# Performance work log

Measured on AMD Instinct MI355X. Metric: run time of the kernel, lower is better.

## Reference

```python
import jax, jax.numpy as jnp
import numpy as np

H = 1024
V = 32000
L = 15
B = 512


def setup_inputs() -> dict:
    key = jax.random.key(0)
    ks = jax.random.split(key, 16)
    s = 0.02
    return {
        "input_ids": jax.random.randint(ks[0], (B,), 0, V),
        "hidden": jax.random.normal(ks[1], (1, B, H), jnp.float32),
        "encoder_outputs": jax.random.normal(ks[2], (L, B, H), jnp.float32),
        "max_length": L,
        "embedding": jax.random.normal(ks[3], (V, H), jnp.float32) * s,
        "attn1_w": jax.random.normal(ks[4], (1, 2 * H), jnp.float32) * s,
        "attn1_b": jnp.zeros((1,), jnp.float32),
        "combine_w": jax.random.normal(ks[5], (H, 2 * H), jnp.float32) * s,
        "combine_b": jnp.zeros((H,), jnp.float32),
        "w_ih": jax.random.normal(ks[6], (3 * H, H), jnp.float32) * s,
        "w_hh": jax.random.normal(ks[7], (3 * H, H), jnp.float32) * s,
        "b_ih": jnp.zeros((3 * H,), jnp.float32),
        "b_hh": jnp.zeros((3 * H,), jnp.float32),
        "out_w": jax.random.normal(ks[8], (V, H), jnp.float32) * s,
        "out_b": jnp.zeros((V,), jnp.float32),
    }


def reference(input_ids, hidden, encoder_outputs, max_length, embedding,
              attn1_w, attn1_b, combine_w, combine_b,
              w_ih, w_hh, b_ih, b_hh, out_w, out_b):
    # embedding lookup (dropout is identity in eval mode)
    emb = embedding[input_ids]                       # [B, H]
    # Bahdanau-style additive scores: vectorize the per-step python loop
    emb_l = jnp.broadcast_to(emb[None], (max_length, B, H))   # [L, B, H]
    cat = jnp.concatenate([emb_l, encoder_outputs], axis=-1)  # [L, B, 2H]
    scores = cat @ attn1_w.T + attn1_b               # [L, B, 1]
    attn_weights = jax.nn.softmax(scores, axis=0)    # softmax over L
    ctx = jnp.sum(attn_weights * encoder_outputs, axis=0)     # [B, H]
    x = jnp.concatenate([emb, ctx], axis=-1) @ combine_w.T + combine_b  # [B, H]
    # n_layers = 1: relu then one GRU step (seq len 1)
    x = jax.nn.relu(x)
    h = hidden[0]                                    # [B, H]
    gi = x @ w_ih.T + b_ih                           # [B, 3H]
    gh = h @ w_hh.T + b_hh                           # [B, 3H]
    i_r, i_z, i_n = jnp.split(gi, 3, axis=1)
    h_r, h_z, h_n = jnp.split(gh, 3, axis=1)
    r = jax.nn.sigmoid(i_r + h_r)
    z = jax.nn.sigmoid(i_z + h_z)
    n = jnp.tanh(i_n + r * h_n)
    h_new = (1.0 - z) * n + z * h                    # [B, H]
    logits = h_new @ out_w.T + out_b                 # [B, V]
    output = jax.nn.log_softmax(logits, axis=1)
    return output, h_new[None], attn_weights
```

## Files before the change

### kernel.cpp

```cpp
#include <hip/hip_runtime.h>

#define HH 1024
#define VV 32000
#define LL 15
#define BB 512

typedef __bf16 bf16;
typedef __bf16 bf16x4 __attribute__((ext_vector_type(4)));
typedef __bf16 bf16x8 __attribute__((ext_vector_type(8)));
typedef float f32x4 __attribute__((ext_vector_type(4)));

__device__ __forceinline__ unsigned short f2bf(float f) {
    unsigned int u = __float_as_uint(f);
    unsigned int r = (u + 0x7fffu + ((u >> 16) & 1u)) >> 16;
    return (unsigned short)r;
}

__device__ __forceinline__ void gld_lds16(const void* g, void* l) {
    __builtin_amdgcn_global_load_lds(
        (const __attribute__((address_space(1))) unsigned int*)g,
        (__attribute__((address_space(3))) unsigned int*)l, 16, 0, 0);
}

__global__ __launch_bounds__(256)
void cvt4_kernel(const float* __restrict__ a0, unsigned short* __restrict__ o0, int n0_,
                 const float* __restrict__ a1, unsigned short* __restrict__ o1, int n1_,
                 const float* __restrict__ a2, unsigned short* __restrict__ o2, int n2_,
                 const float* __restrict__ a3, unsigned short* __restrict__ o3, int n3_) {
    int i = blockIdx.x * 256 + threadIdx.x;
    const float* src; unsigned short* dst;
    if (i < n0_) { src = a0; dst = o0; }
    else if ((i -= n0_) < n1_) { src = a1; dst = o1; }
    else if ((i -= n1_) < n2_) { src = a2; dst = o2; }
    else if ((i -= n2_) < n3_) { src = a3; dst = o3; }
    else return;
    const f32x4 a = ((const f32x4*)src)[2 * i], b = ((const f32x4*)src)[2 * i + 1];
    ((bf16x4*)dst)[2 * i]     = __builtin_convertvector(a, bf16x4);
    ((bf16x4*)dst)[2 * i + 1] = __builtin_convertvector(b, bf16x4);
}

__global__ __launch_bounds__(256)
void attn_kernel(const int* __restrict__ ids, const float* __restrict__ enc,
                 const float* __restrict__ embedding,
                 const float* __restrict__ attn1_w, const float* __restrict__ attn1_b,
                 float* __restrict__ attn_out, unsigned short* __restrict__ cat_out) {
    const int b = blockIdx.x, tid = threadIdx.x;
    const int lane = tid & 63, wv = tid >> 6;

    __shared__ float s_enc[LL * HH];
    __shared__ float s_scores[LL];
    __shared__ float s_red[4];

    for (int idx = tid; idx < LL * HH / 4; idx += 256) {
        const int l = (idx * 4) >> 10, h = (idx * 4) & (HH - 1);
        *(f32x4*)&s_enc[idx * 4] = *(const f32x4*)&enc[((size_t)l * BB + b) * HH + h];
    }

    const float* embr = embedding + (size_t)ids[b] * HH;
    float p = 0.f;
    for (int j = tid; j < HH; j += 256) p += embr[j] * attn1_w[j];
    #pragma unroll
    for (int o = 32; o; o >>= 1) p += __shfl_xor(p, o);
    if (lane == 0) s_red[wv] = p;
    __syncthreads();
    const float semb = s_red[0] + s_red[1] + s_red[2] + s_red[3] + attn1_b[0];

    for (int l = wv; l < LL; l += 4) {
        float q = 0.f;
        for (int j = lane; j < HH; j += 64) q += s_enc[l * HH + j] * attn1_w[HH + j];
        #pragma unroll
        for (int o = 32; o; o >>= 1) q += __shfl_xor(q, o);
        if (lane == 0) s_scores[l] = q + semb;
    }
    __syncthreads();

    float mx = -3.4e38f;
    #pragma unroll
    for (int l = 0; l < LL; l++) mx = fmaxf(mx, s_scores[l]);
    float aw[LL], sum = 0.f;
    #pragma unroll
    for (int l = 0; l < LL; l++) { aw[l] = __expf(s_scores[l] - mx); sum += aw[l]; }
    const float inv = 1.f / sum;
    #pragma unroll
    for (int l = 0; l < LL; l++) aw[l] *= inv;

    if (tid < LL) attn_out[tid * BB + b] = aw[tid];

    for (int j = tid; j < HH; j += 256) {
        float c = 0.f;
        #pragma unroll
        for (int l = 0; l < LL; l++) c += aw[l] * s_enc[l * HH + j];
        cat_out[(size_t)b * (2 * HH) + j] = f2bf(embr[j]);
        cat_out[(size_t)b * (2 * HH) + HH + j] = f2bf(c);
    }
}

template<int TM, int TN, int OUT, int GATES>
__global__ __launch_bounds__(256)
void gemm_nt(const bf16* __restrict__ A, const bf16* __restrict__ B,
             const float* __restrict__ bias, void* __restrict__ Cout,
             const bf16* __restrict__ A2, const bf16* __restrict__ B2,
             const float* __restrict__ bias2, void* __restrict__ C2,
             const int K, const int N) {
    constexpr int FM = TM / 32, FN = TN / 32;
    __shared__ bf16 As[TM * 64];
    __shared__ bf16 Bs[TN * 64];

    if (GATES && blockIdx.z == 1) { A = A2; B = B2; bias = bias2; Cout = C2; }

    const int tid = threadIdx.x;
    const int lane = tid & 63, wave = tid >> 6;
    const int wm = wave >> 1, wn = wave & 1;
    const int rlo = lane & 15, khi = lane >> 4;
    const int m0 = blockIdx.y * TM, n0 = blockIdx.x * TN;

    f32x4 acc[FM][FN] = {};
    constexpr int IA = TM / 32, IB = TN / 32;

    for (int k0 = 0; k0 < K; k0 += 64) {
        #pragma unroll
        for (int i = 0; i < IA; i++) {
            const int t = (i * 256 + tid) * 8;
            gld_lds16(A + (size_t)(m0 + (t >> 6)) * K + (k0 + (t & 63)), As + i * 2048 + wave * 512);
        }
        #pragma unroll
        for (int i = 0; i < IB; i++) {
            const int t = (i * 256 + tid) * 8;
            gld_lds16(B + (size_t)(n0 + (t >> 6)) * K + (k0 + (t & 63)), Bs + i * 2048 + wave * 512);
        }
        __syncthreads();

        bf16x8 af[FM][2], bfr[FN][2];
        #pragma unroll
        for (int m = 0; m < FM; m++)
            #pragma unroll
            for (int ks = 0; ks < 2; ks++)
                af[m][ks] = *(const bf16x8*)(As + (wm * (TM / 2) + m * 16 + rlo) * 64 + ks * 32 + khi * 8);
        #pragma unroll
        for (int n = 0; n < FN; n++)
            #pragma unroll
            for (int ks = 0; ks < 2; ks++)
                bfr[n][ks] = *(const bf16x8*)(Bs + (wn * (TN / 2) + n * 16 + rlo) * 64 + ks * 32 + khi * 8);
        #pragma unroll
        for (int ks = 0; ks < 2; ks++)
            #pragma unroll
            for (int m = 0; m < FM; m++)
                #pragma unroll
                for (int n = 0; n < FN; n++)
                    acc[m][n] = __builtin_amdgcn_mfma_f32_16x16x32_bf16(af[m][ks], bfr[n][ks], acc[m][n], 0, 0, 0);
        __syncthreads();
    }

    #pragma unroll
    for (int m = 0; m < FM; m++) {
        const int gr = m0 + wm * (TM / 2) + m * 16 + khi * 4;
        #pragma unroll
        for (int n = 0; n < FN; n++) {
            const int gc = n0 + wn * (TN / 2) + n * 16 + rlo;
            const float bv = bias[gc];
            #pragma unroll
            for (int j = 0; j < 4; j++) {
                float v = acc[m][n][j] + bv;
                if (OUT == 1) {
                    v = fmaxf(v, 0.f);
                    ((unsigned short*)Cout)[(size_t)(gr + j) * N + gc] = f2bf(v);
                } else {
                    ((float*)Cout)[(size_t)(gr + j) * N + gc] = v;
                }
            }
        }
    }
}

__global__ __launch_bounds__(256)
void gemm_out(const bf16* __restrict__ A, const float* __restrict__ B,
              const float* __restrict__ bias, float* __restrict__ C,
              float* __restrict__ pmax, float* __restrict__ psum) {
    constexpr int K = HH, N = VV;
    __shared__ bf16 As[128 * 64];
    __shared__ char BsB[128 * 128] __attribute__((aligned(128)));
    __shared__ float sPm[2][128], sPs[2][128];

    const int tid = threadIdx.x;
    const int lane = tid & 63, wave = tid >> 6;
    const int wm = wave >> 1, wn = wave & 1;
    const int rlo = lane & 15, khi = lane >> 4;

    constexpr int gridN = VV / 128;
    constexpr int nFull = (gridN >> 3) << 5;
    const int bidx = blockIdx.x;
    int g, jm;
    if (bidx < nFull) { const int s = bidx >> 5, rem = bidx & 31; jm = rem >> 3; g = s * 8 + (rem & 7); }
    else { const int rem = bidx - nFull; constexpr int gleft = gridN & 7; g = (gridN & ~7) + rem % gleft; jm = rem / gleft; }
    const int n0 = g * 128, m0 = jm * 128;

    f32x4 acc[4][4] = {};

    for (int k0 = 0; k0 < K; k0 += 64) {
        #pragma unroll
        for (int i = 0; i < 4; i++) {
            const int t = (i * 256 + tid) * 8;
            gld_lds16(A + (size_t)(m0 + (t >> 6)) * K + (k0 + (t & 63)), As + i * 2048 + wave * 512);
        }
        f32x4 bv[8];
        #pragma unroll
        for (int i = 0; i < 8; i++) {
            const int idx = i * 256 + tid;
            const int row = idx >> 4, c4 = idx & 15;
            bv[i] = *(const f32x4*)(B + (size_t)(n0 + row) * K + k0 + c4 * 4);
        }
        #pragma unroll
        for (int i = 0; i < 8; i++) {
            const int idx = i * 256 + tid;
            const int row = idx >> 4;
            bf16x4 w = __builtin_convertvector(bv[i], bf16x4);
            *(bf16x4*)(BsB + ((idx * 8) ^ ((row & 7) << 4))) = w;
        }
        __syncthreads();

        bf16x8 af[4][2], bfr[4][2];
        #pragma unroll
        for (int m = 0; m < 4; m++)
            #pragma unroll
            for (int ks = 0; ks < 2; ks++)
                af[m][ks] = *(const bf16x8*)(As + (wm * 64 + m * 16 + rlo) * 64 + ks * 32 + khi * 8);
        #pragma unroll
        for (int n = 0; n < 4; n++) {
            const int row = wn * 64 + n * 16 + rlo;
            #pragma unroll
            for (int ks = 0; ks < 2; ks++)
                bfr[n][ks] = *(const bf16x8*)(BsB + ((row * 128 + ks * 64 + khi * 16) ^ ((row & 7) << 4)));
        }
        #pragma unroll
        for (int ks = 0; ks < 2; ks++)
            #pragma unroll
            for (int m = 0; m < 4; m++)
                #pragma unroll
                for (int n = 0; n < 4; n++)
                    acc[m][n] = __builtin_amdgcn_mfma_f32_16x16x32_bf16(af[m][ks], bfr[n][ks], acc[m][n], 0, 0, 0);
        __syncthreads();
    }

    float bvn[4];
    #pragma unroll
    for (int n = 0; n < 4; n++) bvn[n] = bias[n0 + wn * 64 + n * 16 + rlo];

    #pragma unroll
    for (int m = 0; m < 4; m++) {
        const int rbase = wm * 64 + m * 16 + khi * 4;
        #pragma unroll
        for (int j = 0; j < 4; j++) {
            const int gr = m0 + rbase + j;
            float v[4];
            float lm = -3.4e38f;
            #pragma unroll
            for (int n = 0; n < 4; n++) {
                v[n] = acc[m][n][j] + bvn[n];
                C[(size_t)gr * N + n0 + wn * 64 + n * 16 + rlo] = v[n];
                lm = fmaxf(lm, v[n]);
            }
            #pragma unroll
            for (int o = 8; o; o >>= 1) lm = fmaxf(lm, __shfl_xor(lm, o));
            float ls = 0.f;
            #pragma unroll
            for (int n = 0; n < 4; n++) ls += __expf(v[n] - lm);
            #pragma unroll
            for (int o = 8; o; o >>= 1) ls += __shfl_xor(ls, o);
            if (rlo == 0) { sPm[wn][rbase + j] = lm; sPs[wn][rbase + j] = ls; }
        }
    }
    __syncthreads();
    if (tid < 128) {
        const float ma = sPm[0][tid], mb = sPm[1][tid];
        const float M = fmaxf(ma, mb);
        const float S = sPs[0][tid] * __expf(ma - M) + sPs[1][tid] * __expf(mb - M);
        pmax[(size_t)(m0 + tid) * 256 + g] = M;
        psum[(size_t)(m0 + tid) * 256 + g] = S;
    }
}

__global__ __launch_bounds__(256)
void gru_kernel(const float* __restrict__ gi, const float* __restrict__ gh,
                const float* __restrict__ h, float* __restrict__ hnew,
                unsigned short* __restrict__ hnew_bf) {
    const int i = blockIdx.x * 256 + threadIdx.x;
    const int e = i * 4;
    const int b = e >> 10, j = e & (HH - 1);
    const size_t o = ((size_t)b * 3 * HH + j) / 4;
    const f32x4 ir = ((const f32x4*)gi)[o],          iz = ((const f32x4*)gi)[o + HH / 4],
                in_ = ((const f32x4*)gi)[o + 2 * HH / 4];
    const f32x4 hr = ((const f32x4*)gh)[o],          hz = ((const f32x4*)gh)[o + HH / 4],
                hn = ((const f32x4*)gh)[o + 2 * HH / 4];
    const f32x4 hv = ((const f32x4*)h)[i];
    f32x4 out;
    ushort4 ob;
    #pragma unroll
    for (int c = 0; c < 4; c++) {
        const float r = 1.f / (1.f + __expf(-(ir[c] + hr[c])));
        const float z = 1.f / (1.f + __expf(-(iz[c] + hz[c])));
        const float n = tanhf(in_[c] + r * hn[c]);
        const float v = (1.f - z) * n + z * hv[c];
        out[c] = v;
        ((unsigned short*)&ob)[c] = f2bf(v);
    }
    ((f32x4*)hnew)[i] = out;
    ((ushort4*)hnew_bf)[i] = ob;
}

__global__ __launch_bounds__(256)
void lsm_final(const float* __restrict__ pmax, const float* __restrict__ psum,
               float* __restrict__ logits) {
    const int b = blockIdx.x, tid = threadIdx.x;
    const int lane = tid & 63, wv = tid >> 6;
    __shared__ float sm[4], ss[4];

    float m = -3.4e38f, s = 0.f;
    if (tid < VV / 128) { m = pmax[(size_t)b * 256 + tid]; s = psum[(size_t)b * 256 + tid]; }
    #pragma unroll
    for (int o = 32; o; o >>= 1) {
        const float mo = __shfl_xor(m, o), so = __shfl_xor(s, o);
        const float nm = fmaxf(m, mo);
        s = s * __expf(m - nm) + so * __expf(mo - nm);
        m = nm;
    }
    if (lane == 0) { sm[wv] = m; ss[wv] = s; }
    __syncthreads();
    const float M = fmaxf(fmaxf(sm[0], sm[1]), fmaxf(sm[2], sm[3]));
    const float S = ss[0] * __expf(sm[0] - M) + ss[1] * __expf(sm[1] - M)
                  + ss[2] * __expf(sm[2] - M) + ss[3] * __expf(sm[3] - M);
    const float lse = M + __logf(S);

    float* row = logits + (size_t)b * VV;
    for (int j = tid; j < VV / 4; j += 256) {
        f32x4 v = ((const f32x4*)row)[j];
        v[0] -= lse; v[1] -= lse; v[2] -= lse; v[3] -= lse;
        ((f32x4*)row)[j] = v;
    }
}

extern "C" void kernel_launch(void* const* d_in, const int* in_sizes, int n_in,
                              void* d_out, int out_size, void* d_ws, size_t ws_size,
                              hipStream_t stream) {
    const int*   ids       = (const int*)d_in[0];
    const float* hidden    = (const float*)d_in[1];
    const float* enc       = (const float*)d_in[2];
    const float* embedding = (const float*)d_in[4];
    const float* attn1_w   = (const float*)d_in[5];
    const float* attn1_b   = (const float*)d_in[6];
    const float* combine_w = (const float*)d_in[7];
    const float* combine_b = (const float*)d_in[8];
    const float* w_ih      = (const float*)d_in[9];
    const float* w_hh      = (const float*)d_in[10];
    const float* b_ih      = (const float*)d_in[11];
    const float* b_hh      = (const float*)d_in[12];
    const float* out_w     = (const float*)d_in[13];
    const float* out_b     = (const float*)d_in[14];

    float* out_lsm = (float*)d_out;
    float* out_h   = out_lsm + (size_t)BB * VV;
    float* out_aw  = out_h + (size_t)BB * HH;

    char* w = (char*)d_ws;
    unsigned short* w_ih_bf  = (unsigned short*)w;   w += (size_t)3 * HH * HH * 2;
    unsigned short* w_hh_bf  = (unsigned short*)w;   w += (size_t)3 * HH * HH * 2;
    unsigned short* w_cb_bf  = (unsigned short*)w;   w += (size_t)2 * HH * HH * 2;
    unsigned short* cat_bf   = (unsigned short*)w;   w += (size_t)BB * 2 * HH * 2;
    unsigned short* x_bf     = (unsigned short*)w;   w += (size_t)BB * HH * 2;
    unsigned short* hid_bf   = (unsigned short*)w;   w += (size_t)BB * HH * 2;
    unsigned short* hnew_bf  = (unsigned short*)w;   w += (size_t)BB * HH * 2;
    float* gi   = (float*)w;                         w += (size_t)BB * 3 * HH * 4;
    float* gh   = (float*)w;                         w += (size_t)BB * 3 * HH * 4;
    float* pmax = (float*)w;                         w += (size_t)BB * 256 * 4;
    float* psum = (float*)w;                         w += (size_t)BB * 256 * 4;

    cvt4_kernel<<<(3 * HH * HH / 8 * 2 + 2 * HH * HH / 8 + BB * HH / 8) / 256, 256, 0, stream>>>(
        w_ih, w_ih_bf, 3 * HH * HH / 8,
        w_hh, w_hh_bf, 3 * HH * HH / 8,
        combine_w, w_cb_bf, 2 * HH * HH / 8,
        hidden, hid_bf, BB * HH / 8);

    attn_kernel<<<BB, 256, 0, stream>>>(ids, enc, embedding, attn1_w, attn1_b, out_aw, cat_bf);

    gemm_nt<64, 64, 1, 0><<<dim3(HH / 64, BB / 64), 256, 0, stream>>>(
        (const bf16*)cat_bf, (const bf16*)w_cb_bf, combine_b, x_bf,
        nullptr, nullptr, nullptr, nullptr, 2 * HH, HH);

    gemm_nt<64, 64, 0, 1><<<dim3(3 * HH / 64, BB / 64, 2), 256, 0, stream>>>(
        (const bf16*)hid_bf, (const bf16*)w_hh_bf, b_hh, gh,
        (const bf16*)x_bf, (const bf16*)w_ih_bf, b_ih, gi, HH, 3 * HH);

    gru_kernel<<<(BB * HH / 4) / 256, 256, 0, stream>>>(gi, gh, hidden, out_h, hnew_bf);

    gemm_out<<<(VV / 128) * 4, 256, 0, stream>>>(
        (const bf16*)hnew_bf, out_w, out_b, out_lsm, pmax, psum);

    lsm_final<<<BB, 256, 0, stream>>>(pmax, psum, out_lsm);
}
```

Baseline: 186.0 us.

## Halve output GEMM N-tile to 64, swizzle A in LDS, widen softmax reduction

The vocabulary projection GEMM now uses 128x64 tiles instead of 128x128, which doubles the block count to 2000 and cuts per-thread accumulators, and it sets launch bounds to allow 3 blocks per CU. The A tile is now loaded into LDS with an XOR swizzle so fragment reads avoid bank conflicts. The partial max/sum buffers and the final log-softmax kernel are widened to 500 partials per row, using 512 threads. The aim is better occupancy and load balance on the largest GEMM, at the cost of re-reading the A tile twice as often and converting each fp32 weight tile from global memory with less reuse.

```diff
diff --git a/kernel.cpp b/kernel.cpp
--- a/kernel.cpp
+++ b/kernel.cpp
@@ -172,13 +172,13 @@
     }
 }
 
-__global__ __launch_bounds__(256)
+__global__ __launch_bounds__(256, 3)
 void gemm_out(const bf16* __restrict__ A, const float* __restrict__ B,
               const float* __restrict__ bias, float* __restrict__ C,
               float* __restrict__ pmax, float* __restrict__ psum) {
     constexpr int K = HH, N = VV;
     __shared__ bf16 As[128 * 64];
-    __shared__ char BsB[128 * 128] __attribute__((aligned(128)));
+    __shared__ bf16 Bs[64 * 64];
     __shared__ float sPm[2][128], sPs[2][128];
 
     const int tid = threadIdx.x;
@@ -186,64 +186,68 @@
     const int wm = wave >> 1, wn = wave & 1;
     const int rlo = lane & 15, khi = lane >> 4;
 
-    constexpr int gridN = VV / 128;
+    constexpr int gridN = VV / 64;
     constexpr int nFull = (gridN >> 3) << 5;
     const int bidx = blockIdx.x;
     int g, jm;
     if (bidx < nFull) { const int s = bidx >> 5, rem = bidx & 31; jm = rem >> 3; g = s * 8 + (rem & 7); }
     else { const int rem = bidx - nFull; constexpr int gleft = gridN & 7; g = (gridN & ~7) + rem % gleft; jm = rem / gleft; }
-    const int n0 = g * 128, m0 = jm * 128;
-
-    f32x4 acc[4][4] = {};
+    const int n0 = g * 64, m0 = jm * 128;
+
+    f32x4 acc[4][2] = {};
 
     for (int k0 = 0; k0 < K; k0 += 64) {
+        f32x4 bv[4];
         #pragma unroll
         for (int i = 0; i < 4; i++) {
-            const int t = (i * 256 + tid) * 8;
-            gld_lds16(A + (size_t)(m0 + (t >> 6)) * K + (k0 + (t & 63)), As + i * 2048 + wave * 512);
-        }
-        f32x4 bv[8];
-        #pragma unroll
-        for (int i = 0; i < 8; i++) {
             const int idx = i * 256 + tid;
             const int row = idx >> 4, c4 = idx & 15;
             bv[i] = *(const f32x4*)(B + (size_t)(n0 + row) * K + k0 + c4 * 4);
         }
         #pragma unroll
-        for (int i = 0; i < 8; i++) {
+        for (int i = 0; i < 4; i++) {
+            const int p = (i * 256 + tid) * 16;
+            const int row = p >> 7;
+            const int qs = (p & 127) ^ ((row & 7) << 4);
+            gld_lds16(A + (size_t)(m0 + row) * K + k0 + (qs >> 1),
+                      As + i * 2048 + wave * 512);
+        }
+        #pragma unroll
+        for (int i = 0; i < 4; i++) {
             const int idx = i * 256 + tid;
-            const int row = idx >> 4;
+            const int row = idx >> 4, c4 = idx & 15;
             bf16x4 w = __builtin_convertvector(bv[i], bf16x4);
-            *(bf16x4*)(BsB + ((idx * 8) ^ ((row & 7) << 4))) = w;
+            *(bf16x4*)((char*)Bs + row * 128 + ((c4 * 8) ^ ((row & 7) << 4))) = w;
         }
         __syncthreads();
 
-        bf16x8 af[4][2], bfr[4][2];
-        #pragma unroll
-        for (int m = 0; m < 4; m++)
-            #pragma unroll
-            for (int ks = 0; ks < 2; ks++)
-                af[m][ks] = *(const bf16x8*)(As + (wm * 64 + m * 16 + rlo) * 64 + ks * 32 + khi * 8);
-        #pragma unroll
-        for (int n = 0; n < 4; n++) {
-            const int row = wn * 64 + n * 16 + rlo;
-            #pragma unroll
-            for (int ks = 0; ks < 2; ks++)
-                bfr[n][ks] = *(const bf16x8*)(BsB + ((row * 128 + ks * 64 + khi * 16) ^ ((row & 7) << 4)));
-        }
-        #pragma unroll
-        for (int ks = 0; ks < 2; ks++)
+        #pragma unroll
+        for (int ks = 0; ks < 2; ks++) {
+            bf16x8 af[4], bfr[2];
+            #pragma unroll
+            for (int m = 0; m < 4; m++) {
+                const int r = wm * 64 + m * 16 + rlo;
+                const int sw = (ks * 64 + khi * 16) ^ ((r & 7) << 4);
+                af[m] = *(const bf16x8*)((const char*)As + r * 128 + sw);
+            }
+            #pragma unroll
+            for (int n = 0; n < 2; n++) {
+                const int r = wn * 32 + n * 16 + rlo;
+                const int sw = (ks * 64 + khi * 16) ^ ((r & 7) << 4);
+                bfr[n] = *(const bf16x8*)((const char*)Bs + r * 128 + sw);
+            }
             #pragma unroll
             for (int m = 0; m < 4; m++)
                 #pragma unroll
-                for (int n = 0; n < 4; n++)
-                    acc[m][n] = __builtin_amdgcn_mfma_f32_16x16x32_bf16(af[m][ks], bfr[n][ks], acc[m][n], 0, 0, 0);
+                for (int n = 0; n < 2; n++)
+                    acc[m][n] = __builtin_amdgcn_mfma_f32_16x16x32_bf16(af[m], bfr[n], acc[m][n], 0, 0, 0);
+        }
         __syncthreads();
     }
 
-    float bvn[4];
-    #pragma unroll
-    for (int n = 0; n < 4; n++) bvn[n] = bias[n0 + wn * 64 + n * 16 + rlo];
+    float bvn[2];
+    #pragma unroll
+    for (int n = 0; n < 2; n++) bvn[n] = bias[n0 + wn * 32 + n * 16 + rlo];
 
     #pragma unroll
     for (int m = 0; m < 4; m++) {
@@ -251,19 +255,16 @@
         #pragma unroll
         for (int j = 0; j < 4; j++) {
             const int gr = m0 + rbase + j;
-            float v[4];
-            float lm = -3.4e38f;
-            #pragma unroll
-            for (int n = 0; n < 4; n++) {
+            float v[2];
+            #pragma unroll
+            for (int n = 0; n < 2; n++) {
                 v[n] = acc[m][n][j] + bvn[n];
-                C[(size_t)gr * N + n0 + wn * 64 + n * 16 + rlo] = v[n];
-                lm = fmaxf(lm, v[n]);
+                C[(size_t)gr * N + n0 + wn * 32 + n * 16 + rlo] = v[n];
             }
+            float lm = fmaxf(v[0], v[1]);
             #pragma unroll
             for (int o = 8; o; o >>= 1) lm = fmaxf(lm, __shfl_xor(lm, o));
-            float ls = 0.f;
-            #pragma unroll
-            for (int n = 0; n < 4; n++) ls += __expf(v[n] - lm);
+            float ls = __expf(v[0] - lm) + __expf(v[1] - lm);
             #pragma unroll
             for (int o = 8; o; o >>= 1) ls += __shfl_xor(ls, o);
             if (rlo == 0) { sPm[wn][rbase + j] = lm; sPs[wn][rbase + j] = ls; }
@@ -274,8 +275,8 @@
         const float ma = sPm[0][tid], mb = sPm[1][tid];
         const float M = fmaxf(ma, mb);
         const float S = sPs[0][tid] * __expf(ma - M) + sPs[1][tid] * __expf(mb - M);
-        pmax[(size_t)(m0 + tid) * 256 + g] = M;
-        psum[(size_t)(m0 + tid) * 256 + g] = S;
+        pmax[(size_t)(m0 + tid) * 512 + g] = M;
+        psum[(size_t)(m0 + tid) * 512 + g] = S;
     }
 }
 
@@ -307,15 +308,15 @@
     ((ushort4*)hnew_bf)[i] = ob;
 }
 
-__global__ __launch_bounds__(256)
+__global__ __launch_bounds__(512)
 void lsm_final(const float* __restrict__ pmax, const float* __restrict__ psum,
                float* __restrict__ logits) {
     const int b = blockIdx.x, tid = threadIdx.x;
     const int lane = tid & 63, wv = tid >> 6;
-    __shared__ float sm[4], ss[4];
+    __shared__ float sm[8], ss[8];
 
     float m = -3.4e38f, s = 0.f;
-    if (tid < VV / 128) { m = pmax[(size_t)b * 256 + tid]; s = psum[(size_t)b * 256 + tid]; }
+    if (tid < VV / 64) { m = pmax[(size_t)b * 512 + tid]; s = psum[(size_t)b * 512 + tid]; }
     #pragma unroll
     for (int o = 32; o; o >>= 1) {
         const float mo = __shfl_xor(m, o), so = __shfl_xor(s, o);
@@ -325,13 +326,16 @@
     }
     if (lane == 0) { sm[wv] = m; ss[wv] = s; }
     __syncthreads();
-    const float M = fmaxf(fmaxf(sm[0], sm[1]), fmaxf(sm[2], sm[3]));
-    const float S = ss[0] * __expf(sm[0] - M) + ss[1] * __expf(sm[1] - M)
-                  + ss[2] * __expf(sm[2] - M) + ss[3] * __expf(sm[3] - M);
+    float M = sm[0], S;
+    #pragma unroll
+    for (int w = 1; w < 8; w++) M = fmaxf(M, sm[w]);
+    S = ss[0] * __expf(sm[0] - M);
+    #pragma unroll
+    for (int w = 1; w < 8; w++) S += ss[w] * __expf(sm[w] - M);
     const float lse = M + __logf(S);
 
     float* row = logits + (size_t)b * VV;
-    for (int j = tid; j < VV / 4; j += 256) {
+    for (int j = tid; j < VV / 4; j += 512) {
         f32x4 v = ((const f32x4*)row)[j];
         v[0] -= lse; v[1] -= lse; v[2] -= lse; v[3] -= lse;
         ((f32x4*)row)[j] = v;
@@ -370,8 +374,8 @@
     unsigned short* hnew_bf  = (unsigned short*)w;   w += (size_t)BB * HH * 2;
     float* gi   = (float*)w;                         w += (size_t)BB * 3 * HH * 4;
     float* gh   = (float*)w;                         w += (size_t)BB * 3 * HH * 4;
-    float* pmax = (float*)w;                         w += (size_t)BB * 256 * 4;
-    float* psum = (float*)w;                         w += (size_t)BB * 256 * 4;
+    float* pmax = (float*)w;                         w += (size_t)BB * 512 * 4;
+    float* psum = (float*)w;                         w += (size_t)BB * 512 * 4;
 
     cvt4_kernel<<<(3 * HH * HH / 8 * 2 + 2 * HH * HH / 8 + BB * HH / 8) / 256, 256, 0, stream>>>(
         w_ih, w_ih_bf, 3 * HH * HH / 8,
@@ -391,8 +395,8 @@
 
     gru_kernel<<<(BB * HH / 4) / 256, 256, 0, stream>>>(gi, gh, hidden, out_h, hnew_bf);
 
-    gemm_out<<<(VV / 128) * 4, 256, 0, stream>>>(
+    gemm_out<<<(VV / 64) * 4, 256, 0, stream>>>(
         (const bf16*)hnew_bf, out_w, out_b, out_lsm, pmax, psum);
 
-    lsm_final<<<BB, 256, 0, stream>>>(pmax, psum, out_lsm);
-}
+    lsm_final<<<BB, 512, 0, stream>>>(pmax, psum, out_lsm);
+}
```

After: 183.0 us. Within noise of the previous version (-1.6%).
